# Performance work log

Measured on AMD Instinct MI355X. Metric: run time of the kernel, lower is better.

Reference implementation:

```python
import jax, jax.numpy as jnp
import numpy as np

D_MODEL = 1024
NUM_HEADS = 16
D_K = D_MODEL // NUM_HEADS
SCALE = float(np.sqrt(D_K))


def setup_inputs() -> dict:
    key = jax.random.key(0)
    ks = jax.random.split(key, 11)
    B, S, D = 2, 2048, D_MODEL
    def lin(kw):
        # xavier-uniform-ish weight, zero bias (matches torch init style)
        lim = float(np.sqrt(6.0 / (D + D)))
        return jax.random.uniform(kw, (D, D), jnp.float32, -lim, lim)
    return {
        "q": jax.random.normal(ks[0], (B, S, D), jnp.float32),
        "k": jax.random.normal(ks[1], (B, S, D), jnp.float32),
        "v": jax.random.normal(ks[2], (B, S, D), jnp.float32),
        "Wq": lin(ks[3]), "bq": jnp.zeros((D,), jnp.float32),
        "Wk": lin(ks[4]), "bk": jnp.zeros((D,), jnp.float32),
        "Wv": lin(ks[5]), "bv": jnp.zeros((D,), jnp.float32),
        "Wo": lin(ks[6]), "bo": jnp.zeros((D,), jnp.float32),
    }


def _split_heads(x):
    B, S, _ = x.shape
    return x.reshape(B, S, NUM_HEADS, D_K).transpose(0, 2, 1, 3)  # (B,H,S,dk)


def reference(q, k, v, Wq, bq, Wk, bk, Wv, bv, Wo, bo):
    # torch nn.Linear: y = x @ W.T + b
    Q = _split_heads(q @ Wq.T + bq)
    K = _split_heads(k @ Wk.T + bk)
    V = _split_heads(v @ Wv.T + bv)
    scores = jnp.einsum("bhqd,bhkd->bhqk", Q, K) / SCALE
    # numerically-stable softmax with detached max (as in the torch code)
    m = jax.lax.stop_gradient(jnp.max(scores, axis=-1, keepdims=True))
    exp_scores = jnp.exp(scores - m)
    attn = exp_scores / (jnp.sum(exp_scores, axis=-1, keepdims=True) + 1e-9)
    out = jnp.einsum("bhqk,bhkd->bhqd", attn, V)  # (B,H,S,dk)
    B, H, S, dk = out.shape
    out = out.transpose(0, 2, 1, 3).reshape(B, S, H * dk)
    return out @ Wo.T + bo
```

## Files before the change

### kernel.cpp

```cpp
#include <hip/hip_runtime.h>


#define D_MODEL 1024
#define NHEADS  16
#define DKH     64
#define SEQ     2048
#define BATCH   2
#define MTOT    (BATCH * SEQ)
#define XE      ((long)MTOT * D_MODEL)
#define WE      ((long)D_MODEL * D_MODEL)
#define QSCALE  0.18033688011112042f

typedef __attribute__((ext_vector_type(8))) short short8v;
typedef __attribute__((ext_vector_type(4))) short short4v;
typedef __attribute__((ext_vector_type(4))) float f32x4;

typedef __attribute__((address_space(1))) void as1_void;
typedef __attribute__((address_space(3))) void as3_void;

__device__ __forceinline__ void gload16(const void* g, void* l) {
    __builtin_amdgcn_global_load_lds((const as1_void*)g, (as3_void*)l, 16, 0, 0);
}

__device__ __forceinline__ unsigned short f2bf(float x) {
    unsigned int u = __float_as_uint(x);
    u += 0x7FFFu + ((u >> 16) & 1u);
    return (unsigned short)(u >> 16);
}

__device__ __forceinline__ float fexp2(float x) {
    return __builtin_amdgcn_exp2f(x);
}

__device__ __forceinline__ unsigned int cvt_pk_bf16(float lo, float hi) {
    unsigned int r;
    asm("v_cvt_pk_bf16_f32 %0, %1, %2" : "=v"(r) : "v"(lo), "v"(hi));
    return r;
}

__device__ __forceinline__ int swz_u(int row, int col) {
    int byte = (col << 1) ^ ((row & 7) << 4);
    return (row << 6) + (byte >> 1);
}

__device__ __forceinline__ int swz_v(int d, int kv) {
    int slot = (d & 6) | ((d >> 3) & 1);
    int byte = (kv << 1) ^ (slot << 4);
    return (d << 6) + (byte >> 1);
}

struct ConvArgs {
    const float*    src[4];
    unsigned short* dst[4];
    int             n4[4];
};

__global__ __launch_bounds__(256) void convert_kernel(ConvArgs a) {
    int z = blockIdx.y;
    const float4*   s = (const float4*)a.src[z];
    unsigned short* d = a.dst[z];
    int n = a.n4[z];
    for (int i = blockIdx.x * blockDim.x + threadIdx.x; i < n;
         i += gridDim.x * blockDim.x) {
        float4 v = s[i];
        ushort4 o;
        o.x = f2bf(v.x); o.y = f2bf(v.y); o.z = f2bf(v.z); o.w = f2bf(v.w);
        *(ushort4*)(d + 4L * i) = o;
    }
}

#define PBM 256
#define PBK 64
#define PTILE (PBM * PBK)

__global__ __launch_bounds__(512) void proj_kernel(
    const float* __restrict__ xq, const float* __restrict__ xk,
    const float* __restrict__ xv, const unsigned short* __restrict__ wb,
    const float* __restrict__ bq, const float* __restrict__ bk,
    const float* __restrict__ bv, unsigned short* __restrict__ qkv) {
    __shared__ unsigned short As[2 * PTILE];
    __shared__ unsigned short Bs[2 * PTILE];

    const int t    = threadIdx.x;
    const int lane = t & 63;
    const int w    = t >> 6;
    const int wm   = w >> 2, wn = w & 3;
    const int l15  = lane & 15, g = lane >> 4;

    const int bid = blockIdx.x;
    const int xcd = bid & 7;
    const int k   = bid >> 3;
    const int ty  = (xcd << 1) | (k & 1);
    const int tx  = (k >> 1) & 3;
    const int z   = k >> 3;
    const float* bias = (z == 0) ? bq : (z == 1) ? bk : bv;
    const float scale = (z == 0) ? QSCALE : 1.0f;

    const float* Af = (z == 0) ? xq : (z == 1) ? xk : xv;
    const unsigned short* Bm = wb + (long)z * WE;
    unsigned short*       C  = qkv + (long)z * XE;
    const long m0 = (long)ty * PBM;
    const long n0 = (long)tx * PBM;
    const int  K  = D_MODEL;

    f32x4 acc[8][4] = {};

    int srow[4], scol[4];
#pragma unroll
    for (int c = 0; c < 4; ++c) {
        int idx = t + c * 512;
        srow[c] = idx >> 3;
        scol[c] = ((idx & 7) ^ (srow[c] & 7)) * 8;
    }

    float4 a0_[4], a1_[4];

#define PLOAD_A(k0)                                                        \
    _Pragma("unroll")                                                      \
    for (int c = 0; c < 4; ++c) {                                          \
        const float* src = Af + (m0 + srow[c]) * K + (k0) + scol[c];       \
        a0_[c] = *(const float4*)(src);                                    \
        a1_[c] = *(const float4*)(src + 4);                                \
    }

#define PSTAGE_B(k0, buf)                                                  \
    _Pragma("unroll")                                                      \
    for (int c = 0; c < 4; ++c) {                                          \
        int idx = t + c * 512;                                             \
        gload16(Bm + (n0 + srow[c]) * K + (k0) + scol[c],                  \
                &Bs[(buf) * PTILE + idx * 8]);                             \
    }

#define PWRITE_A(buf)                                                      \
    _Pragma("unroll")                                                      \
    for (int c = 0; c < 4; ++c) {                                          \
        int idx = t + c * 512;                                             \
        uint4 pk;                                                          \
        pk.x = cvt_pk_bf16(a0_[c].x, a0_[c].y);                            \
        pk.y = cvt_pk_bf16(a0_[c].z, a0_[c].w);                            \
        pk.z = cvt_pk_bf16(a1_[c].x, a1_[c].y);                            \
        pk.w = cvt_pk_bf16(a1_[c].z, a1_[c].w);                            \
        *(uint4*)&As[(buf) * PTILE + idx * 8] = pk;                        \
    }

    PLOAD_A(0);
    PSTAGE_B(0, 0);
    PWRITE_A(0);
    int cur = 0;

    for (int it = 0; it < K / PBK; ++it) {
        const int nxt = cur ^ 1;
        const int kn  = ((it + 1) * PBK) & (K - 1);
        PLOAD_A(kn);
        PSTAGE_B(kn, nxt);
        asm volatile("s_waitcnt vmcnt(12)" ::: "memory");
        asm volatile("s_waitcnt lgkmcnt(0)" ::: "memory");
        __builtin_amdgcn_sched_barrier(0);
        __builtin_amdgcn_s_barrier();
        __builtin_amdgcn_sched_barrier(0);

        const unsigned short* Ab = &As[cur * PTILE];
        const unsigned short* Bb = &Bs[cur * PTILE];

#pragma unroll
        for (int kk = 0; kk < 2; ++kk) {
            short8v bf_[4];
#pragma unroll
            for (int nf = 0; nf < 4; ++nf) {
                int r = wn * 64 + nf * 16 + l15;
                bf_[nf] = *(const short8v*)&Bb[r * 64 + (((kk * 4 + g) ^ (r & 7)) * 8)];
            }
#pragma unroll
            for (int mh = 0; mh < 2; ++mh) {
                short8v af_[4];
#pragma unroll
                for (int i = 0; i < 4; ++i) {
                    int r = wm * 128 + (mh * 4 + i) * 16 + l15;
                    af_[i] = *(const short8v*)&Ab[r * 64 + (((kk * 4 + g) ^ (r & 7)) * 8)];
                }
                __builtin_amdgcn_s_setprio(1);
#pragma unroll
                for (int i = 0; i < 4; ++i)
#pragma unroll
                    for (int nf = 0; nf < 4; ++nf)
                        acc[mh * 4 + i][nf] = __builtin_amdgcn_mfma_f32_16x16x32_bf16(
                            af_[i], bf_[nf], acc[mh * 4 + i][nf], 0, 0, 0);
                __builtin_amdgcn_s_setprio(0);
            }
        }

        asm volatile("s_waitcnt lgkmcnt(0)" ::: "memory");
        __builtin_amdgcn_sched_barrier(0);
        __builtin_amdgcn_s_barrier();
        __builtin_amdgcn_sched_barrier(0);

        PWRITE_A(nxt);
        cur = nxt;
    }

    float bvv[4];
#pragma unroll
    for (int nf = 0; nf < 4; ++nf)
        bvv[nf] = bias[n0 + wn * 64 + nf * 16 + l15];

#pragma unroll
    for (int mf = 0; mf < 8; ++mf)
#pragma unroll
        for (int nf = 0; nf < 4; ++nf)
#pragma unroll
            for (int r = 0; r < 4; ++r) {
                long row = m0 + wm * 128 + mf * 16 + g * 4 + r;
                long col = n0 + wn * 64 + nf * 16 + l15;
                C[row * (long)D_MODEL + col] =
                    f2bf((acc[mf][nf][r] + bvv[nf]) * scale);
            }
#undef PLOAD_A
#undef PSTAGE_B
#undef PWRITE_A
}

__global__ __launch_bounds__(256) void out_kernel(
    const unsigned short* __restrict__ ob, const unsigned short* __restrict__ wo,
    const float* __restrict__ bo, float* __restrict__ out) {
    __shared__ unsigned short As[128 * 32];
    __shared__ unsigned short Bs[128 * 32];

    const int t    = threadIdx.x;
    const int lane = t & 63;
    const int w    = t >> 6;
    const int wm   = w >> 1, wn = w & 1;
    const int l15  = lane & 15, g = lane >> 4;

    const int bid = blockIdx.x;
    const int xcd = bid & 7;
    const int k   = bid >> 3;
    const long m0 = (long)((xcd << 2) | (k & 3)) * 128;
    const long n0 = (long)(k >> 2) * 128;
    const int  K  = D_MODEL, N = D_MODEL;

    f32x4 acc[4][4] = {};

    const int idx0 = t, idx1 = t + 256;
    const int r0 = idx0 >> 2, c0 = (idx0 & 3) * 8;
    const int r1 = idx1 >> 2, c1 = (idx1 & 3) * 8;
    const unsigned short* pa0 = ob + (m0 + r0) * K + c0;
    const unsigned short* pa1 = ob + (m0 + r1) * K + c1;
    const unsigned short* pb0 = wo + (n0 + r0) * K + c0;
    const unsigned short* pb1 = wo + (n0 + r1) * K + c1;

    for (int k0 = 0; k0 < K; k0 += 32) {
        gload16(pa0 + k0, &As[idx0 * 8]);
        gload16(pa1 + k0, &As[idx1 * 8]);
        gload16(pb0 + k0, &Bs[idx0 * 8]);
        gload16(pb1 + k0, &Bs[idx1 * 8]);
        __syncthreads();

        short8v af[4], bf_[4];
#pragma unroll
        for (int mf = 0; mf < 4; ++mf)
            af[mf] = *(const short8v*)&As[(wm * 64 + mf * 16 + l15) * 32 + g * 8];
#pragma unroll
        for (int nf = 0; nf < 4; ++nf)
            bf_[nf] = *(const short8v*)&Bs[(wn * 64 + nf * 16 + l15) * 32 + g * 8];
#pragma unroll
        for (int mf = 0; mf < 4; ++mf)
#pragma unroll
            for (int nf = 0; nf < 4; ++nf)
                acc[mf][nf] = __builtin_amdgcn_mfma_f32_16x16x32_bf16(
                    af[mf], bf_[nf], acc[mf][nf], 0, 0, 0);
        __syncthreads();
    }

    float bvv[4];
#pragma unroll
    for (int nf = 0; nf < 4; ++nf)
        bvv[nf] = bo[n0 + wn * 64 + nf * 16 + l15];

#pragma unroll
    for (int mf = 0; mf < 4; ++mf)
#pragma unroll
        for (int nf = 0; nf < 4; ++nf)
#pragma unroll
            for (int r = 0; r < 4; ++r) {
                long row = m0 + wm * 64 + mf * 16 + g * 4 + r;
                long col = n0 + wn * 64 + nf * 16 + l15;
                out[row * (long)N + col] = acc[mf][nf][r] + bvv[nf];
            }
}

#define KVB 4096

__global__ __launch_bounds__(512) void attn_kernel(
    const unsigned short* __restrict__ Qb, const unsigned short* __restrict__ Kb,
    const unsigned short* __restrict__ Vb, unsigned short* __restrict__ Ob) {
    __shared__ alignas(16) unsigned short Ks[2 * KVB];
    __shared__ alignas(16) unsigned short Vt[2 * KVB];
    __shared__ alignas(16) unsigned short Ps[8][16 * 64];
    __shared__ alignas(16) float corrS[8][16];

    const int t = threadIdx.x, lane = t & 63, w = t >> 6;
    const int l15 = lane & 15, g = lane >> 4;
    const int bid = blockIdx.x;
    const int xcd = bid & 7;
    const int kk2 = bid >> 3;
    const int bh  = (xcd << 2) | (kk2 & 3);
    const int qb  = kk2 >> 2;
    const long headoff = (long)(bh >> 4) * SEQ * D_MODEL + (long)(bh & 15) * DKH;
    const int q0w = qb * 128 + w * 16;

    short8v qf[2];
#pragma unroll
    for (int ks = 0; ks < 2; ++ks)
        qf[ks] = *(const short8v*)(Qb + headoff +
            (long)(q0w + l15) * D_MODEL + ks * 32 + g * 8);

    short8v onesv;
#pragma unroll
    for (int j = 0; j < 8; ++j) onesv[j] = (short)0x3F80;

    f32x4 o[4] = {};
    f32x4 ol = {};
    float mrun = -3.0e38f;

    const int vd0  = (t & 31) * 2;
    const int vkv0 = (t >> 5) * 4;
    const int kr0 = t >> 3, ks0 = t & 7;

    unsigned int va[4];

#define ISSUE_V(kt)                                                        \
    _Pragma("unroll")                                                      \
    for (int j = 0; j < 4; ++j)                                            \
        va[j] = *(const unsigned int*)(Vb + headoff +                      \
            (long)((kt) + vkv0 + j) * D_MODEL + vd0);

#define ISSUE_K(kt, off)                                                   \
    gload16(Kb + headoff + (long)((kt) + kr0) * D_MODEL +                  \
                ((ks0 ^ (kr0 & 7)) << 3), &Ks[(off) + t * 8]);

#define WRITE_V(off)                                                       \
    {                                                                      \
        short4v ra, rb;                                                    \
        _Pragma("unroll")                                                  \
        for (int j = 0; j < 4; ++j) {                                      \
            ra[j] = (short)(va[j] & 0xffffu);                              \
            rb[j] = (short)(va[j] >> 16);                                  \
        }                                                                  \
        *(short4v*)&Vt[(off) + swz_v(vd0,     vkv0)] = ra;                 \
        *(short4v*)&Vt[(off) + swz_v(vd0 + 1, vkv0)] = rb;                 \
    }

    asm volatile("s_waitcnt vmcnt(0)" ::: "memory");
    ISSUE_V(0);
    ISSUE_K(0, 0);
    WRITE_V(0);
    int cur = 0;

    for (int it = 0; it < SEQ / 64; ++it) {
        const int nxt = cur ^ 1;
        const int ktn = (((it + 1) & (SEQ / 64 - 1))) * 64;
        ISSUE_V(ktn);
        ISSUE_K(ktn, nxt * KVB);
        asm volatile("s_waitcnt vmcnt(5)" ::: "memory");
        asm volatile("s_waitcnt lgkmcnt(0)" ::: "memory");
        __builtin_amdgcn_sched_barrier(0);
        __builtin_amdgcn_s_barrier();
        __builtin_amdgcn_sched_barrier(0);

        const int kO = cur * KVB;

        f32x4 st[4] = {};
        __builtin_amdgcn_s_setprio(1);
#pragma unroll
        for (int ks = 0; ks < 2; ++ks)
#pragma unroll
            for (int mf = 0; mf < 4; ++mf) {
                short8v kf = *(const short8v*)&Ks[kO + swz_u(mf * 16 + l15, ks * 32 + g * 8)];
                st[mf] = __builtin_amdgcn_mfma_f32_16x16x32_bf16(
                    kf, qf[ks], st[mf], 0, 0, 0);
            }
        __builtin_amdgcn_s_setprio(0);

        float vmax = st[0][0];
#pragma unroll
        for (int mf = 0; mf < 4; ++mf)
#pragma unroll
            for (int r = 0; r < 4; ++r)
                vmax = fmaxf(vmax, st[mf][r]);
        vmax = fmaxf(vmax, __shfl_xor(vmax, 16));
        vmax = fmaxf(vmax, __shfl_xor(vmax, 32));

        const bool grow = __any(vmax > mrun + 8.0f);
        if (grow) {
            float mnew = fmaxf(mrun, vmax);
            float corr = fexp2(mrun - mnew);
            mrun = mnew;
            if (g == 0) corrS[w][l15] = corr;
        }

#pragma unroll
        for (int mf = 0; mf < 4; ++mf)
#pragma unroll
            for (int r = 0; r < 4; ++r)
                st[mf][r] = fexp2(st[mf][r] - mrun);

        unsigned short* Pw = Ps[w];
#pragma unroll
        for (int mf = 0; mf < 4; ++mf) {
            uint2 pk;
            pk.x = cvt_pk_bf16(st[mf][0], st[mf][1]);
            pk.y = cvt_pk_bf16(st[mf][2], st[mf][3]);
            *(uint2*)&Pw[swz_u(l15, mf * 16 + g * 4)] = pk;
        }

        if (grow) {
            float4 cv = *(const float4*)&corrS[w][g * 4];
#pragma unroll
            for (int nd = 0; nd < 4; ++nd)
#pragma unroll
                for (int r = 0; r < 4; ++r)
                    o[nd][r] *= cv[r];
#pragma unroll
            for (int r = 0; r < 4; ++r) ol[r] *= cv[r];
        }

        __builtin_amdgcn_s_setprio(1);
#pragma unroll
        for (int ks2 = 0; ks2 < 2; ++ks2) {
            short8v pf = *(const short8v*)&Pw[swz_u(l15, ks2 * 32 + g * 8)];
            ol = __builtin_amdgcn_mfma_f32_16x16x32_bf16(
                pf, onesv, ol, 0, 0, 0);
#pragma unroll
            for (int nd = 0; nd < 4; ++nd) {
                short8v vf = *(const short8v*)&Vt[kO + swz_v(nd * 16 + l15, ks2 * 32 + g * 8)];
                o[nd] = __builtin_amdgcn_mfma_f32_16x16x32_bf16(
                    pf, vf, o[nd], 0, 0, 0);
            }
        }
        __builtin_amdgcn_s_setprio(0);

        WRITE_V(nxt * KVB);
        cur = nxt;
    }

#pragma unroll
    for (int r = 0; r < 4; ++r) {
        float inv = 1.f / (ol[r] + 1e-9f);
        long rowoff = headoff + (long)(q0w + g * 4 + r) * D_MODEL;
#pragma unroll
        for (int nd = 0; nd < 4; ++nd)
            Ob[rowoff + nd * 16 + l15] = f2bf(o[nd][r] * inv);
    }
#undef ISSUE_V
#undef ISSUE_K
#undef WRITE_V
}

extern "C" void kernel_launch(void* const* d_in, const int* in_sizes, int n_in,
                              void* d_out, int out_size, void* d_ws, size_t ws_size,
                              hipStream_t stream) {
    unsigned short* ws  = (unsigned short*)d_ws;
    unsigned short* wb  = ws;
    unsigned short* qkv = ws + 4L * WE;
    unsigned short* ob  = qkv + 3L * XE;

    ConvArgs ca;
    ca.src[0] = (const float*)d_in[3]; ca.dst[0] = wb;           ca.n4[0] = (int)(WE / 4);
    ca.src[1] = (const float*)d_in[5]; ca.dst[1] = wb + WE;      ca.n4[1] = (int)(WE / 4);
    ca.src[2] = (const float*)d_in[7]; ca.dst[2] = wb + 2L * WE; ca.n4[2] = (int)(WE / 4);
    ca.src[3] = (const float*)d_in[9]; ca.dst[3] = wb + 3L * WE; ca.n4[3] = (int)(WE / 4);

    hipLaunchKernelGGL(convert_kernel, dim3(512, 4), dim3(256), 0, stream, ca);

    hipLaunchKernelGGL(proj_kernel, dim3(192), dim3(512), 0, stream,
                       (const float*)d_in[0], (const float*)d_in[1],
                       (const float*)d_in[2], wb,
                       (const float*)d_in[4], (const float*)d_in[6],
                       (const float*)d_in[8], qkv);

    hipLaunchKernelGGL(attn_kernel, dim3(512), dim3(512), 0, stream,
                       qkv, qkv + XE, qkv + 2L * XE, ob);

    hipLaunchKernelGGL(out_kernel, dim3(256), dim3(256), 0, stream,
                       ob, wb + 3L * WE, (const float*)d_in[10], (float*)d_out);
}
```

Baseline: 129.2 us.

## Shrink QKV projection tiles to 128x128x32 with 256-thread blocks and more blocks

Changes the projection GEMM from 256x256 tiles with BK=64 and 512 threads to 128x128 tiles with BK=32 and 256 threads, launching 768 blocks instead of 192. It also drops the XOR swizzle on the LDS layout. The goal is better occupancy and load balance across the CUs, since 192 large blocks underfill the GPU. In exchange each tile reuses less data, global traffic per FLOP goes up, and the unswizzled LDS reads may hit bank conflicts.

```diff
diff --git a/kernel.cpp b/kernel.cpp
--- a/kernel.cpp
+++ b/kernel.cpp
@@ -69,78 +69,71 @@
     }
 }
 
-#define PBM 256
-#define PBK 64
-#define PTILE (PBM * PBK)
-
-__global__ __launch_bounds__(512) void proj_kernel(
+__global__ __launch_bounds__(256) void proj_kernel(
     const float* __restrict__ xq, const float* __restrict__ xk,
     const float* __restrict__ xv, const unsigned short* __restrict__ wb,
     const float* __restrict__ bq, const float* __restrict__ bk,
     const float* __restrict__ bv, unsigned short* __restrict__ qkv) {
-    __shared__ unsigned short As[2 * PTILE];
-    __shared__ unsigned short Bs[2 * PTILE];
+    __shared__ unsigned short As[2 * 128 * 32];
+    __shared__ unsigned short Bs[2 * 128 * 32];
 
     const int t    = threadIdx.x;
     const int lane = t & 63;
     const int w    = t >> 6;
-    const int wm   = w >> 2, wn = w & 3;
+    const int wm   = w >> 1, wn = w & 1;
     const int l15  = lane & 15, g = lane >> 4;
 
     const int bid = blockIdx.x;
     const int xcd = bid & 7;
     const int k   = bid >> 3;
-    const int ty  = (xcd << 1) | (k & 1);
-    const int tx  = (k >> 1) & 3;
-    const int z   = k >> 3;
+    const int ty  = (xcd << 2) | (k & 3);
+    const int tx  = (k >> 2) & 7;
+    const int z   = k >> 5;
     const float* bias = (z == 0) ? bq : (z == 1) ? bk : bv;
     const float scale = (z == 0) ? QSCALE : 1.0f;
 
     const float* Af = (z == 0) ? xq : (z == 1) ? xk : xv;
     const unsigned short* Bm = wb + (long)z * WE;
     unsigned short*       C  = qkv + (long)z * XE;
-    const long m0 = (long)ty * PBM;
-    const long n0 = (long)tx * PBM;
+    const long m0 = (long)ty * 128;
+    const long n0 = (long)tx * 128;
     const int  K  = D_MODEL;
 
-    f32x4 acc[8][4] = {};
-
-    int srow[4], scol[4];
-#pragma unroll
-    for (int c = 0; c < 4; ++c) {
-        int idx = t + c * 512;
-        srow[c] = idx >> 3;
-        scol[c] = ((idx & 7) ^ (srow[c] & 7)) * 8;
-    }
-
-    float4 a0_[4], a1_[4];
+    f32x4 acc[4][4] = {};
+
+    const int idx0 = t, idx1 = t + 256;
+    const int r0 = idx0 >> 2, c0 = (idx0 & 3) * 8;
+    const int r1 = idx1 >> 2, c1 = (idx1 & 3) * 8;
+
+    float4 a0_[2], a1_[2];
 
 #define PLOAD_A(k0)                                                        \
-    _Pragma("unroll")                                                      \
-    for (int c = 0; c < 4; ++c) {                                          \
-        const float* src = Af + (m0 + srow[c]) * K + (k0) + scol[c];       \
-        a0_[c] = *(const float4*)(src);                                    \
-        a1_[c] = *(const float4*)(src + 4);                                \
+    {                                                                      \
+        const float* s0 = Af + (m0 + r0) * K + (k0) + c0;                  \
+        const float* s1 = Af + (m0 + r1) * K + (k0) + c1;                  \
+        a0_[0] = *(const float4*)(s0);                                     \
+        a1_[0] = *(const float4*)(s0 + 4);                                 \
+        a0_[1] = *(const float4*)(s1);                                     \
+        a1_[1] = *(const float4*)(s1 + 4);                                 \
     }
 
 #define PSTAGE_B(k0, buf)                                                  \
-    _Pragma("unroll")                                                      \
-    for (int c = 0; c < 4; ++c) {                                          \
-        int idx = t + c * 512;                                             \
-        gload16(Bm + (n0 + srow[c]) * K + (k0) + scol[c],                  \
-                &Bs[(buf) * PTILE + idx * 8]);                             \
-    }
+    gload16(Bm + (n0 + r0) * K + (k0) + c0, &Bs[(buf) * 4096 + idx0 * 8]); \
+    gload16(Bm + (n0 + r1) * K + (k0) + c1, &Bs[(buf) * 4096 + idx1 * 8]);
 
 #define PWRITE_A(buf)                                                      \
-    _Pragma("unroll")                                                      \
-    for (int c = 0; c < 4; ++c) {                                          \
-        int idx = t + c * 512;                                             \
+    {                                                                      \
         uint4 pk;                                                          \
-        pk.x = cvt_pk_bf16(a0_[c].x, a0_[c].y);                            \
-        pk.y = cvt_pk_bf16(a0_[c].z, a0_[c].w);                            \
-        pk.z = cvt_pk_bf16(a1_[c].x, a1_[c].y);                            \
-        pk.w = cvt_pk_bf16(a1_[c].z, a1_[c].w);                            \
-        *(uint4*)&As[(buf) * PTILE + idx * 8] = pk;                        \
+        pk.x = cvt_pk_bf16(a0_[0].x, a0_[0].y);                            \
+        pk.y = cvt_pk_bf16(a0_[0].z, a0_[0].w);                            \
+        pk.z = cvt_pk_bf16(a1_[0].x, a1_[0].y);                            \
+        pk.w = cvt_pk_bf16(a1_[0].z, a1_[0].w);                            \
+        *(uint4*)&As[(buf) * 4096 + idx0 * 8] = pk;                        \
+        pk.x = cvt_pk_bf16(a0_[1].x, a0_[1].y);                            \
+        pk.y = cvt_pk_bf16(a0_[1].z, a0_[1].w);                            \
+        pk.z = cvt_pk_bf16(a1_[1].x, a1_[1].y);                            \
+        pk.w = cvt_pk_bf16(a1_[1].z, a1_[1].w);                            \
+        *(uint4*)&As[(buf) * 4096 + idx1 * 8] = pk;                        \
     }
 
     PLOAD_A(0);
@@ -148,46 +141,35 @@
     PWRITE_A(0);
     int cur = 0;
 
-    for (int it = 0; it < K / PBK; ++it) {
+    for (int it = 0; it < K / 32; ++it) {
         const int nxt = cur ^ 1;
-        const int kn  = ((it + 1) * PBK) & (K - 1);
+        const int kn  = ((it + 1) * 32) & (K - 1);
         PLOAD_A(kn);
         PSTAGE_B(kn, nxt);
-        asm volatile("s_waitcnt vmcnt(12)" ::: "memory");
+        asm volatile("s_waitcnt vmcnt(6)" ::: "memory");
         asm volatile("s_waitcnt lgkmcnt(0)" ::: "memory");
         __builtin_amdgcn_sched_barrier(0);
         __builtin_amdgcn_s_barrier();
         __builtin_amdgcn_sched_barrier(0);
 
-        const unsigned short* Ab = &As[cur * PTILE];
-        const unsigned short* Bb = &Bs[cur * PTILE];
-
-#pragma unroll
-        for (int kk = 0; kk < 2; ++kk) {
-            short8v bf_[4];
-#pragma unroll
-            for (int nf = 0; nf < 4; ++nf) {
-                int r = wn * 64 + nf * 16 + l15;
-                bf_[nf] = *(const short8v*)&Bb[r * 64 + (((kk * 4 + g) ^ (r & 7)) * 8)];
-            }
-#pragma unroll
-            for (int mh = 0; mh < 2; ++mh) {
-                short8v af_[4];
-#pragma unroll
-                for (int i = 0; i < 4; ++i) {
-                    int r = wm * 128 + (mh * 4 + i) * 16 + l15;
-                    af_[i] = *(const short8v*)&Ab[r * 64 + (((kk * 4 + g) ^ (r & 7)) * 8)];
-                }
-                __builtin_amdgcn_s_setprio(1);
-#pragma unroll
-                for (int i = 0; i < 4; ++i)
-#pragma unroll
-                    for (int nf = 0; nf < 4; ++nf)
-                        acc[mh * 4 + i][nf] = __builtin_amdgcn_mfma_f32_16x16x32_bf16(
-                            af_[i], bf_[nf], acc[mh * 4 + i][nf], 0, 0, 0);
-                __builtin_amdgcn_s_setprio(0);
-            }
-        }
+        const unsigned short* Ab = &As[cur * 4096];
+        const unsigned short* Bb = &Bs[cur * 4096];
+
+        short8v af[4], bf_[4];
+#pragma unroll
+        for (int mf = 0; mf < 4; ++mf)
+            af[mf] = *(const short8v*)&Ab[(wm * 64 + mf * 16 + l15) * 32 + g * 8];
+#pragma unroll
+        for (int nf = 0; nf < 4; ++nf)
+            bf_[nf] = *(const short8v*)&Bb[(wn * 64 + nf * 16 + l15) * 32 + g * 8];
+        __builtin_amdgcn_s_setprio(1);
+#pragma unroll
+        for (int mf = 0; mf < 4; ++mf)
+#pragma unroll
+            for (int nf = 0; nf < 4; ++nf)
+                acc[mf][nf] = __builtin_amdgcn_mfma_f32_16x16x32_bf16(
+                    af[mf], bf_[nf], acc[mf][nf], 0, 0, 0);
+        __builtin_amdgcn_s_setprio(0);
 
         asm volatile("s_waitcnt lgkmcnt(0)" ::: "memory");
         __builtin_amdgcn_sched_barrier(0);
@@ -204,12 +186,12 @@
         bvv[nf] = bias[n0 + wn * 64 + nf * 16 + l15];
 
 #pragma unroll
-    for (int mf = 0; mf < 8; ++mf)
+    for (int mf = 0; mf < 4; ++mf)
 #pragma unroll
         for (int nf = 0; nf < 4; ++nf)
 #pragma unroll
             for (int r = 0; r < 4; ++r) {
-                long row = m0 + wm * 128 + mf * 16 + g * 4 + r;
+                long row = m0 + wm * 64 + mf * 16 + g * 4 + r;
                 long col = n0 + wn * 64 + nf * 16 + l15;
                 C[row * (long)D_MODEL + col] =
                     f2bf((acc[mf][nf][r] + bvv[nf]) * scale);
@@ -472,7 +454,7 @@
 
     hipLaunchKernelGGL(convert_kernel, dim3(512, 4), dim3(256), 0, stream, ca);
 
-    hipLaunchKernelGGL(proj_kernel, dim3(192), dim3(512), 0, stream,
+    hipLaunchKernelGGL(proj_kernel, dim3(768), dim3(256), 0, stream,
                        (const float*)d_in[0], (const float*)d_in[1],
                        (const float*)d_in[2], wb,
                        (const float*)d_in[4], (const float*)d_in[6],
```

Result: no change. 127.7 us, median of 7 (-1.2%).
